# Kernel tuning notes

Measured on AMD Instinct MI355X. Metric: run time of the kernel, lower is better.

Reference implementation:

```python
import jax, jax.numpy as jnp
import numpy as np

B, T, C, H = 8, 2048, 2048, 128  # batch, seq, n_embd, head_size


def setup_inputs() -> dict:
    key = jax.random.key(0)
    kx, kq, kk, kv = jax.random.split(key, 4)
    x = jax.random.normal(kx, (B, T, C), dtype=jnp.float32)
    # Linear(n_embd, head_size, bias=False); stored as [in, out] so x @ W matches x @ weight.T in torch
    Wq = jax.random.normal(kq, (C, H), dtype=jnp.float32) * 0.02
    Wk = jax.random.normal(kk, (C, H), dtype=jnp.float32) * 0.02
    Wv = jax.random.normal(kv, (C, H), dtype=jnp.float32) * 0.02
    return {"x": x, "Wq": Wq, "Wk": Wk, "Wv": Wv}


def reference(x, Wq, Wk, Wv):
    # Single-head scaled dot-product attention (mask=False path of the module)
    q = jnp.einsum("btc,ch->bth", x, Wq)  # [B,T,H]
    k = jnp.einsum("btc,ch->bth", x, Wk)
    v = jnp.einsum("btc,ch->bth", x, Wv)
    scale = k.shape[-1] ** -0.5
    wei = jnp.einsum("bqh,bkh->bqk", q, k) * scale  # [B,T,T]
    wei = jax.nn.softmax(wei, axis=-1)
    out = jnp.einsum("bqk,bkh->bqh", wei, v)  # [B,T,H]
    return out
```

## Files before the change

### kernel.cpp

```cpp
#include <hip/hip_runtime.h>
#include <hip/hip_bf16.h>

typedef __attribute__((ext_vector_type(8))) short short8;
typedef __attribute__((ext_vector_type(4))) float f32x4;

#define MFMA16(a, b, c) __builtin_amdgcn_mfma_f32_16x16x32_bf16((a), (b), (c), 0, 0, 0)

__device__ __forceinline__ unsigned short f2bf(float f) {
    __hip_bfloat16 h = __float2bfloat16(f);
    return __builtin_bit_cast(unsigned short, h);
}

__device__ __forceinline__ short8 cvt8(f32x4 a, f32x4 b) {
    short8 r;
    r[0] = (short)f2bf(a[0]); r[1] = (short)f2bf(a[1]);
    r[2] = (short)f2bf(a[2]); r[3] = (short)f2bf(a[3]);
    r[4] = (short)f2bf(b[0]); r[5] = (short)f2bf(b[1]);
    r[6] = (short)f2bf(b[2]); r[7] = (short)f2bf(b[3]);
    return r;
}

__global__ __launch_bounds__(256) void wt_kernel(const float* __restrict__ Wq,
                                                 const float* __restrict__ Wk,
                                                 const float* __restrict__ Wv,
                                                 unsigned short* __restrict__ Wt) {
    __shared__ float T[64][65];
    const int j = blockIdx.z;
    const float* W = (j == 0) ? Wq : (j == 1) ? Wk : Wv;
    const int c0 = blockIdx.x * 64;
    const int h0 = blockIdx.y * 64;
    const int tid = threadIdx.x;

#pragma unroll
    for (int i = 0; i < 4; i++) {
        const int cc = tid + 256 * i;
        const int r = cc >> 4;
        const int q4 = (cc & 15) * 4;
        f32x4 vv = *(const f32x4*)(W + (size_t)(c0 + r) * 128 + h0 + q4);
        T[r][q4 + 0] = vv[0]; T[r][q4 + 1] = vv[1];
        T[r][q4 + 2] = vv[2]; T[r][q4 + 3] = vv[3];
    }
    __syncthreads();
#pragma unroll
    for (int i = 0; i < 2; i++) {
        const int oc = tid + 256 * i;
        const int hr = oc >> 3;
        const int c8 = (oc & 7) * 8;
        short8 r;
#pragma unroll
        for (int e = 0; e < 8; e++) r[e] = (short)f2bf(T[c8 + e][hr]);
        *(short8*)(Wt + (size_t)j * (128 * 2048) + (size_t)(h0 + hr) * 2048 + c0 + c8) = r;
    }
}

__global__ __launch_bounds__(256) void qkv_gemm(const float* __restrict__ x,
                                                const unsigned short* __restrict__ Wt,
                                                unsigned short* __restrict__ qkv) {
    constexpr int LDT = 72;
    __shared__ __align__(16) unsigned short As[128 * LDT];
    __shared__ __align__(16) unsigned short Bs[128 * LDT];

    const int tid = threadIdx.x;
    const int l = tid & 63;
    const int w = tid >> 6;
    const int wr = w >> 1, wc = w & 1;
    const int bn = blockIdx.x;
    const int bm = blockIdx.y;
    const int lrow = l & 15, lk = (l >> 4) * 8;

    const float* xA = x + (size_t)bm * 128 * 2048;
    const unsigned short* Wb = Wt + (size_t)bn * (128 * 2048);
    unsigned short* outp = qkv + (size_t)bn * (16384 * 128);

    const f32x4 fzero = {0.f, 0.f, 0.f, 0.f};
    f32x4 acc[4][4];
#pragma unroll
    for (int mt = 0; mt < 4; mt++)
#pragma unroll
        for (int nt = 0; nt < 4; nt++) acc[mt][nt] = fzero;

    for (int kt = 0; kt < 32; kt++) {
        __syncthreads();
#pragma unroll
        for (int i = 0; i < 4; i++) {
            const int c = tid + 256 * i;
            const int m = c >> 3;
            const int k0 = (c & 7) * 8;
            const float* src = xA + (size_t)m * 2048 + kt * 64 + k0;
            f32x4 f0 = *(const f32x4*)(src);
            f32x4 f1 = *(const f32x4*)(src + 4);
            *(short8*)&As[m * LDT + k0] = cvt8(f0, f1);
        }
#pragma unroll
        for (int i = 0; i < 4; i++) {
            const int c = tid + 256 * i;
            const int n = c >> 3;
            const int k0 = (c & 7) * 8;
            short8 bv = *(const short8*)(Wb + (size_t)n * 2048 + kt * 64 + k0);
            *(short8*)&Bs[n * LDT + k0] = bv;
        }
        __syncthreads();
#pragma unroll
        for (int ks = 0; ks < 2; ks++) {
            short8 af[4], bfr[4];
#pragma unroll
            for (int mt = 0; mt < 4; mt++)
                af[mt] = *(const short8*)&As[(wr * 64 + mt * 16 + lrow) * LDT + ks * 32 + lk];
#pragma unroll
            for (int nt = 0; nt < 4; nt++)
                bfr[nt] = *(const short8*)&Bs[(wc * 64 + nt * 16 + lrow) * LDT + ks * 32 + lk];
#pragma unroll
            for (int mt = 0; mt < 4; mt++)
#pragma unroll
                for (int nt = 0; nt < 4; nt++)
                    acc[mt][nt] = MFMA16(af[mt], bfr[nt], acc[mt][nt]);
        }
    }

    const float scale = (bn == 0) ? 0.08838834764831845f : 1.0f;
#pragma unroll
    for (int mt = 0; mt < 4; mt++)
#pragma unroll
        for (int nt = 0; nt < 4; nt++)
#pragma unroll
            for (int r = 0; r < 4; r++) {
                const int row = bm * 128 + wr * 64 + mt * 16 + (l >> 4) * 4 + r;
                const int col = wc * 64 + nt * 16 + lrow;
                outp[(size_t)row * 128 + col] = f2bf(acc[mt][nt][r] * scale);
            }
}

template <bool SPLIT>
__global__ __launch_bounds__(256) void attn_kernel_t(const unsigned short* __restrict__ q,
                                                     const unsigned short* __restrict__ k,
                                                     const unsigned short* __restrict__ v,
                                                     float* __restrict__ Oout,
                                                     float* __restrict__ Ml) {
    constexpr int KS = 136;
    constexpr int VS = 88;
    constexpr int PS = 88;
    __shared__ __align__(16) unsigned short Ks[64 * KS];
    __shared__ __align__(16) unsigned short Vt[128 * VS];
    __shared__ __align__(16) unsigned short Psh[64 * PS];

    const int tid = threadIdx.x;
    const int l = tid & 63;
    const int w = tid >> 6;
    const int qt = blockIdx.x;
    const int b = blockIdx.y;
    const int s = SPLIT ? blockIdx.z : 0;
    const int kv_beg = SPLIT ? s * 11 : 0;
    const int kv_end = SPLIT ? ((s == 2) ? 32 : kv_beg + 11) : 32;
    const int lrow = l & 15, g = l >> 4, lk = g * 8;

    const size_t qbase = ((size_t)b * 2048 + qt * 64 + w * 16 + lrow) * 128;
    short8 qf[4];
#pragma unroll
    for (int ks = 0; ks < 4; ks++) qf[ks] = *(const short8*)(q + qbase + ks * 32 + lk);

    const f32x4 fzero = {0.f, 0.f, 0.f, 0.f};
    float m_r[4], l_r[4];
    f32x4 oacc[8];
#pragma unroll
    for (int r = 0; r < 4; r++) { m_r[r] = -1e30f; l_r[r] = 0.f; }
#pragma unroll
    for (int d = 0; d < 8; d++) oacc[d] = fzero;

    const int skey = tid & 63;
    const int sd = (tid >> 6) * 8;

    for (int kv = kv_beg; kv < kv_end; kv++) {
        __syncthreads();
        const size_t kvbase = ((size_t)b * 2048 + kv * 64 + skey) * 128;
#pragma unroll
        for (int jj = 0; jj < 4; jj++) {
            const int d0 = sd + jj * 32;
            short8 kvv = *(const short8*)(k + kvbase + d0);
            *(short8*)&Ks[skey * KS + d0] = kvv;
        }
#pragma unroll
        for (int jj = 0; jj < 4; jj++) {
            const int d0 = sd + jj * 32;
            short8 vv = *(const short8*)(v + kvbase + d0);
#pragma unroll
            for (int e = 0; e < 8; e++)
                Vt[(d0 + e) * VS + skey] = (unsigned short)vv[e];
        }
        __syncthreads();

        f32x4 sv[4];
#pragma unroll
        for (int nt = 0; nt < 4; nt++) sv[nt] = fzero;
#pragma unroll
        for (int ks = 0; ks < 4; ks++)
#pragma unroll
            for (int nt = 0; nt < 4; nt++) {
                short8 kf = *(const short8*)&Ks[(nt * 16 + lrow) * KS + ks * 32 + lk];
                sv[nt] = MFMA16(qf[ks], kf, sv[nt]);
            }

        float sf[4];
#pragma unroll
        for (int r = 0; r < 4; r++) {
            float tmax = fmaxf(fmaxf(sv[0][r], sv[1][r]), fmaxf(sv[2][r], sv[3][r]));
#pragma unroll
            for (int mk = 8; mk >= 1; mk >>= 1) tmax = fmaxf(tmax, __shfl_xor(tmax, mk));
            const float mnew = fmaxf(m_r[r], tmax);
            sf[r] = __expf(m_r[r] - mnew);
            m_r[r] = mnew;
            float psum = 0.f;
#pragma unroll
            for (int nt = 0; nt < 4; nt++) {
                const float p = __expf(sv[nt][r] - mnew);
                sv[nt][r] = p;
                psum += p;
            }
#pragma unroll
            for (int mk = 8; mk >= 1; mk >>= 1) psum += __shfl_xor(psum, mk);
            l_r[r] = l_r[r] * sf[r] + psum;
        }
#pragma unroll
        for (int d = 0; d < 8; d++)
#pragma unroll
            for (int r = 0; r < 4; r++) oacc[d][r] *= sf[r];

#pragma unroll
        for (int nt = 0; nt < 4; nt++)
#pragma unroll
            for (int r = 0; r < 4; r++)
                Psh[(w * 16 + g * 4 + r) * PS + nt * 16 + lrow] = f2bf(sv[nt][r]);
        __syncthreads();

#pragma unroll
        for (int ks2 = 0; ks2 < 2; ks2++) {
            short8 pa = *(const short8*)&Psh[(w * 16 + lrow) * PS + ks2 * 32 + lk];
#pragma unroll
            for (int dt = 0; dt < 8; dt++) {
                short8 vbf = *(const short8*)&Vt[(dt * 16 + lrow) * VS + ks2 * 32 + lk];
                oacc[dt] = MFMA16(pa, vbf, oacc[dt]);
            }
        }
    }

#pragma unroll
    for (int r = 0; r < 4; r++) {
        const int rowi = b * 2048 + qt * 64 + w * 16 + g * 4 + r;
        if (SPLIT) {
            const size_t obase = ((size_t)s * 16384 + rowi) * 128;
#pragma unroll
            for (int dt = 0; dt < 8; dt++)
                Oout[obase + dt * 16 + lrow] = oacc[dt][r];
            if (lrow == 0) {
                const size_t mb = ((size_t)s * 16384 + rowi) * 2;
                Ml[mb] = m_r[r];
                Ml[mb + 1] = l_r[r];
            }
        } else {
            const float inv = 1.0f / l_r[r];
#pragma unroll
            for (int dt = 0; dt < 8; dt++)
                Oout[(size_t)rowi * 128 + dt * 16 + lrow] = oacc[dt][r] * inv;
        }
    }
}

__global__ __launch_bounds__(256) void attn_merge(const float* __restrict__ Oacc,
                                                  const float* __restrict__ Ml,
                                                  float* __restrict__ out) {
    const int row = blockIdx.x * 2 + (threadIdx.x >> 7);
    const int c = threadIdx.x & 127;
    const float m0 = Ml[(size_t)(0 * 16384 + row) * 2], l0 = Ml[(size_t)(0 * 16384 + row) * 2 + 1];
    const float m1 = Ml[(size_t)(1 * 16384 + row) * 2], l1 = Ml[(size_t)(1 * 16384 + row) * 2 + 1];
    const float m2 = Ml[(size_t)(2 * 16384 + row) * 2], l2 = Ml[(size_t)(2 * 16384 + row) * 2 + 1];
    const float M = fmaxf(m0, fmaxf(m1, m2));
    const float w0 = __expf(m0 - M), w1 = __expf(m1 - M), w2 = __expf(m2 - M);
    const float D = w0 * l0 + w1 * l1 + w2 * l2;
    const float o = w0 * Oacc[(size_t)(0 * 16384 + row) * 128 + c] +
                    w1 * Oacc[(size_t)(1 * 16384 + row) * 128 + c] +
                    w2 * Oacc[(size_t)(2 * 16384 + row) * 128 + c];
    out[(size_t)row * 128 + c] = o / D;
}

extern "C" void kernel_launch(void* const* d_in, const int* in_sizes, int n_in,
                              void* d_out, int out_size, void* d_ws, size_t ws_size,
                              hipStream_t stream) {
    const float* x  = (const float*)d_in[0];
    const float* Wq = (const float*)d_in[1];
    const float* Wk = (const float*)d_in[2];
    const float* Wv = (const float*)d_in[3];
    float* out = (float*)d_out;

    unsigned short* ws = (unsigned short*)d_ws;
    unsigned short* qb = ws;
    unsigned short* kb = qb + (size_t)16384 * 128;
    unsigned short* vb = kb + (size_t)16384 * 128;
    unsigned short* Wt = vb + (size_t)16384 * 128;
    float* Oacc = (float*)(Wt + (size_t)3 * 128 * 2048);
    float* Ml = Oacc + (size_t)3 * 16384 * 128;
    const size_t ws_need = (size_t)((char*)(Ml + (size_t)3 * 16384 * 2) - (char*)d_ws);

    hipLaunchKernelGGL(wt_kernel, dim3(32, 2, 3), dim3(256), 0, stream, Wq, Wk, Wv, Wt);
    hipLaunchKernelGGL(qkv_gemm, dim3(3, 128), dim3(256), 0, stream, x, Wt, qb);
    if (ws_size >= ws_need) {
        hipLaunchKernelGGL((attn_kernel_t<true>), dim3(32, 8, 3), dim3(256), 0, stream,
                           qb, kb, vb, Oacc, Ml);
        hipLaunchKernelGGL(attn_merge, dim3(8192), dim3(256), 0, stream, Oacc, Ml, out);
    } else {
        hipLaunchKernelGGL((attn_kernel_t<false>), dim3(32, 8), dim3(256), 0, stream,
                           qb, kb, vb, out, (float*)nullptr);
    }
}
```

Baseline: 295.9 us.

## Double-buffer QKV GEMM with direct global-to-LDS loads and swizzled B tile

Rewrites the QKV projection GEMM to use 64-row M tiles (768 blocks), double-buffered LDS, and prefetch of the next k-tile during MFMA compute. The B tile is loaded with global_load_lds straight into an XOR-swizzled LDS layout, while the fp32 x tile is held in registers and converted to bf16 after compute. It also remaps block IDs so blocks sharing an x row tile are grouped, and sets launch bounds for 3 blocks per CU. The aim is to hide global load latency and cut the per-iteration sync count, at the cost of more LDS and a smaller per-block tile.

Measured after the change: 293.0 us. No clear change (-1.0%).

```diff
diff --git a/kernel.cpp b/kernel.cpp
--- a/kernel.cpp
+++ b/kernel.cpp
@@ -5,6 +5,11 @@
 typedef __attribute__((ext_vector_type(4))) float f32x4;
 
 #define MFMA16(a, b, c) __builtin_amdgcn_mfma_f32_16x16x32_bf16((a), (b), (c), 0, 0, 0)
+
+#define GLOAD_LDS16(gp, lp)                                                            \
+    __builtin_amdgcn_global_load_lds(                                                  \
+        (const __attribute__((address_space(1))) unsigned int*)(gp),                   \
+        (__attribute__((address_space(3))) unsigned int*)(lp), 16, 0, 0)
 
 __device__ __forceinline__ unsigned short f2bf(float f) {
     __hip_bfloat16 h = __float2bfloat16(f);
@@ -53,78 +58,112 @@
     }
 }
 
-__global__ __launch_bounds__(256) void qkv_gemm(const float* __restrict__ x,
-                                                const unsigned short* __restrict__ Wt,
-                                                unsigned short* __restrict__ qkv) {
-    constexpr int LDT = 72;
-    __shared__ __align__(16) unsigned short As[128 * LDT];
-    __shared__ __align__(16) unsigned short Bs[128 * LDT];
+__global__ __launch_bounds__(256, 3) void qkv_gemm(const float* __restrict__ x,
+                                                   const unsigned short* __restrict__ Wt,
+                                                   unsigned short* __restrict__ qkv) {
+    constexpr int LDA = 72;
+    __shared__ __align__(16) unsigned short As[2][64 * LDA];
+    __shared__ __align__(16) unsigned short Bs[2][128 * 64];
 
     const int tid = threadIdx.x;
     const int l = tid & 63;
     const int w = tid >> 6;
     const int wr = w >> 1, wc = w & 1;
-    const int bn = blockIdx.x;
-    const int bm = blockIdx.y;
-    const int lrow = l & 15, lk = (l >> 4) * 8;
-
-    const float* xA = x + (size_t)bm * 128 * 2048;
+    const int lrow = l & 15, g = l >> 4, lk = g * 8;
+
+    const int p = blockIdx.x;
+    const int wg = (p & 7) * 96 + (p >> 3);
+    const int bn = wg % 3;
+    const int bm = wg / 3;
+
+    const float* xA = x + (size_t)bm * 64 * 2048;
     const unsigned short* Wb = Wt + (size_t)bn * (128 * 2048);
     unsigned short* outp = qkv + (size_t)bn * (16384 * 128);
 
+    const int rowA = tid >> 2;
+    const int quad = tid & 3;
+    const float* srcA0 = xA + (size_t)rowA * 2048 + quad * 16;
+
+    const int brow_base = (w << 5) + (l >> 3);
+    const int bsw = ((l >> 3) & 7) << 4;
+    const int bslot = (l & 7) << 4;
+    const int bsrc_off = ((bslot ^ bsw) >> 1);
+
     const f32x4 fzero = {0.f, 0.f, 0.f, 0.f};
-    f32x4 acc[4][4];
-#pragma unroll
-    for (int mt = 0; mt < 4; mt++)
+    f32x4 acc[2][4];
+#pragma unroll
+    for (int mt = 0; mt < 2; mt++)
 #pragma unroll
         for (int nt = 0; nt < 4; nt++) acc[mt][nt] = fzero;
 
+#pragma unroll
+    for (int i = 0; i < 4; i++) {
+        const int row = brow_base + (i << 3);
+        GLOAD_LDS16(Wb + (size_t)row * 2048 + bsrc_off,
+                    &Bs[0][(w << 11) + (i << 9)]);
+    }
+    {
+        f32x4 a0 = *(const f32x4*)(srcA0);
+        f32x4 a1 = *(const f32x4*)(srcA0 + 4);
+        f32x4 a2 = *(const f32x4*)(srcA0 + 8);
+        f32x4 a3 = *(const f32x4*)(srcA0 + 12);
+        *(short8*)&As[0][rowA * LDA + quad * 16] = cvt8(a0, a1);
+        *(short8*)&As[0][rowA * LDA + quad * 16 + 8] = cvt8(a2, a3);
+    }
+    __syncthreads();
+
+    int cur = 0;
     for (int kt = 0; kt < 32; kt++) {
-        __syncthreads();
-#pragma unroll
-        for (int i = 0; i < 4; i++) {
-            const int c = tid + 256 * i;
-            const int m = c >> 3;
-            const int k0 = (c & 7) * 8;
-            const float* src = xA + (size_t)m * 2048 + kt * 64 + k0;
-            f32x4 f0 = *(const f32x4*)(src);
-            f32x4 f1 = *(const f32x4*)(src + 4);
-            *(short8*)&As[m * LDT + k0] = cvt8(f0, f1);
-        }
-#pragma unroll
-        for (int i = 0; i < 4; i++) {
-            const int c = tid + 256 * i;
-            const int n = c >> 3;
-            const int k0 = (c & 7) * 8;
-            short8 bv = *(const short8*)(Wb + (size_t)n * 2048 + kt * 64 + k0);
-            *(short8*)&Bs[n * LDT + k0] = bv;
-        }
-        __syncthreads();
+        f32x4 a0, a1, a2, a3;
+        if (kt < 31) {
+#pragma unroll
+            for (int i = 0; i < 4; i++) {
+                const int row = brow_base + (i << 3);
+                GLOAD_LDS16(Wb + (size_t)row * 2048 + (kt + 1) * 64 + bsrc_off,
+                            &Bs[cur ^ 1][(w << 11) + (i << 9)]);
+            }
+            const float* sA = srcA0 + (kt + 1) * 64;
+            a0 = *(const f32x4*)(sA);
+            a1 = *(const f32x4*)(sA + 4);
+            a2 = *(const f32x4*)(sA + 8);
+            a3 = *(const f32x4*)(sA + 12);
+        }
+
 #pragma unroll
         for (int ks = 0; ks < 2; ks++) {
-            short8 af[4], bfr[4];
-#pragma unroll
-            for (int mt = 0; mt < 4; mt++)
-                af[mt] = *(const short8*)&As[(wr * 64 + mt * 16 + lrow) * LDT + ks * 32 + lk];
-#pragma unroll
-            for (int nt = 0; nt < 4; nt++)
-                bfr[nt] = *(const short8*)&Bs[(wc * 64 + nt * 16 + lrow) * LDT + ks * 32 + lk];
-#pragma unroll
-            for (int mt = 0; mt < 4; mt++)
+            short8 af[2], bfr[4];
+#pragma unroll
+            for (int mt = 0; mt < 2; mt++)
+                af[mt] = *(const short8*)&As[cur][(wr * 32 + mt * 16 + lrow) * LDA + ks * 32 + lk];
+#pragma unroll
+            for (int nt = 0; nt < 4; nt++) {
+                const int n = wc * 64 + nt * 16 + lrow;
+                const int kbyte = (ks * 64 + g * 16) ^ ((n & 7) << 4);
+                bfr[nt] = *(const short8*)&Bs[cur][n * 64 + (kbyte >> 1)];
+            }
+#pragma unroll
+            for (int mt = 0; mt < 2; mt++)
 #pragma unroll
                 for (int nt = 0; nt < 4; nt++)
                     acc[mt][nt] = MFMA16(af[mt], bfr[nt], acc[mt][nt]);
         }
+
+        if (kt < 31) {
+            *(short8*)&As[cur ^ 1][rowA * LDA + quad * 16] = cvt8(a0, a1);
+            *(short8*)&As[cur ^ 1][rowA * LDA + quad * 16 + 8] = cvt8(a2, a3);
+        }
+        __syncthreads();
+        cur ^= 1;
     }
 
     const float scale = (bn == 0) ? 0.08838834764831845f : 1.0f;
 #pragma unroll
-    for (int mt = 0; mt < 4; mt++)
+    for (int mt = 0; mt < 2; mt++)
 #pragma unroll
         for (int nt = 0; nt < 4; nt++)
 #pragma unroll
             for (int r = 0; r < 4; r++) {
-                const int row = bm * 128 + wr * 64 + mt * 16 + (l >> 4) * 4 + r;
+                const int row = bm * 64 + wr * 32 + mt * 16 + g * 4 + r;
                 const int col = wc * 64 + nt * 16 + lrow;
                 outp[(size_t)row * 128 + col] = f2bf(acc[mt][nt][r] * scale);
             }
@@ -211,9 +250,9 @@
             float psum = 0.f;
 #pragma unroll
             for (int nt = 0; nt < 4; nt++) {
-                const float p = __expf(sv[nt][r] - mnew);
-                sv[nt][r] = p;
-                psum += p;
+                const float pp = __expf(sv[nt][r] - mnew);
+                sv[nt][r] = pp;
+                psum += pp;
             }
 #pragma unroll
             for (int mk = 8; mk >= 1; mk >>= 1) psum += __shfl_xor(psum, mk);
@@ -300,7 +339,7 @@
     const size_t ws_need = (size_t)((char*)(Ml + (size_t)3 * 16384 * 2) - (char*)d_ws);
 
     hipLaunchKernelGGL(wt_kernel, dim3(32, 2, 3), dim3(256), 0, stream, Wq, Wk, Wv, Wt);
-    hipLaunchKernelGGL(qkv_gemm, dim3(3, 128), dim3(256), 0, stream, x, Wt, qb);
+    hipLaunchKernelGGL(qkv_gemm, dim3(768), dim3(256), 0, stream, x, Wt, qb);
     if (ws_size >= ws_need) {
         hipLaunchKernelGGL((attn_kernel_t<true>), dim3(32, 8, 3), dim3(256), 0, stream,
                            qb, kb, vb, Oacc, Ml);
```

## Prefetch next K/V tile in attention and stream QKV GEMM operands without LDS

Applied to the files above, without the earlier changes.

The attention kernel now loads the next K/V tile into registers while the current tile's QK^T, softmax and PV run. The tile is written to shared memory after a barrier at the end of each iteration. The barrier between the P write and the P read is dropped, because each wave reads only its own P rows. The QKV projection GEMM drops its shared-memory staging: each wave loads its own fp32 x rows and bf16 weight fragments straight from global memory. Its 2D grid becomes a 1D grid with a swizzle that keeps the three projections of a row block on the same XCD to share L2, and both kernels get a minimum-occupancy launch bound. The risks are higher register pressure and redundant global weight loads across waves, which now rely on cache hits.

After: 407.5 us. 37.7% more time.

```diff
diff --git a/kernel.cpp b/kernel.cpp
--- a/kernel.cpp
+++ b/kernel.cpp
@@ -53,89 +53,73 @@
     }
 }
 
-__global__ __launch_bounds__(256) void qkv_gemm(const float* __restrict__ x,
-                                                const unsigned short* __restrict__ Wt,
-                                                unsigned short* __restrict__ qkv) {
-    constexpr int LDT = 72;
-    __shared__ __align__(16) unsigned short As[128 * LDT];
-    __shared__ __align__(16) unsigned short Bs[128 * LDT];
-
+__global__ __launch_bounds__(256, 3) void qkv_gemm(const float* __restrict__ x,
+                                                   const unsigned short* __restrict__ Wt,
+                                                   unsigned short* __restrict__ qkv) {
     const int tid = threadIdx.x;
     const int l = tid & 63;
     const int w = tid >> 6;
-    const int wr = w >> 1, wc = w & 1;
-    const int bn = blockIdx.x;
-    const int bm = blockIdx.y;
-    const int lrow = l & 15, lk = (l >> 4) * 8;
-
-    const float* xA = x + (size_t)bm * 128 * 2048;
+    const int lrow = l & 15, g = l >> 4;
+
+    const int p = blockIdx.x;
+    const int wg = (p & 7) * 48 + (p >> 3);
+    const int bn = wg % 3;
+    const int bm = wg / 3;
+
     const unsigned short* Wb = Wt + (size_t)bn * (128 * 2048);
     unsigned short* outp = qkv + (size_t)bn * (16384 * 128);
 
+    const float* xb = x + ((size_t)bm * 128 + w * 32 + lrow) * 2048 + g * 8;
+    const unsigned short* wbl = Wb + (size_t)lrow * 2048 + g * 8;
+
     const f32x4 fzero = {0.f, 0.f, 0.f, 0.f};
-    f32x4 acc[4][4];
-#pragma unroll
-    for (int mt = 0; mt < 4; mt++)
-#pragma unroll
-        for (int nt = 0; nt < 4; nt++) acc[mt][nt] = fzero;
-
-    for (int kt = 0; kt < 32; kt++) {
-        __syncthreads();
-#pragma unroll
-        for (int i = 0; i < 4; i++) {
-            const int c = tid + 256 * i;
-            const int m = c >> 3;
-            const int k0 = (c & 7) * 8;
-            const float* src = xA + (size_t)m * 2048 + kt * 64 + k0;
-            f32x4 f0 = *(const f32x4*)(src);
-            f32x4 f1 = *(const f32x4*)(src + 4);
-            *(short8*)&As[m * LDT + k0] = cvt8(f0, f1);
-        }
-#pragma unroll
-        for (int i = 0; i < 4; i++) {
-            const int c = tid + 256 * i;
-            const int n = c >> 3;
-            const int k0 = (c & 7) * 8;
-            short8 bv = *(const short8*)(Wb + (size_t)n * 2048 + kt * 64 + k0);
-            *(short8*)&Bs[n * LDT + k0] = bv;
-        }
-        __syncthreads();
-#pragma unroll
-        for (int ks = 0; ks < 2; ks++) {
-            short8 af[4], bfr[4];
-#pragma unroll
-            for (int mt = 0; mt < 4; mt++)
-                af[mt] = *(const short8*)&As[(wr * 64 + mt * 16 + lrow) * LDT + ks * 32 + lk];
-#pragma unroll
-            for (int nt = 0; nt < 4; nt++)
-                bfr[nt] = *(const short8*)&Bs[(wc * 64 + nt * 16 + lrow) * LDT + ks * 32 + lk];
-#pragma unroll
-            for (int mt = 0; mt < 4; mt++)
-#pragma unroll
-                for (int nt = 0; nt < 4; nt++)
-                    acc[mt][nt] = MFMA16(af[mt], bfr[nt], acc[mt][nt]);
-        }
+    f32x4 acc[2][8];
+#pragma unroll
+    for (int mt = 0; mt < 2; mt++)
+#pragma unroll
+        for (int nt = 0; nt < 8; nt++) acc[mt][nt] = fzero;
+
+#pragma unroll 4
+    for (int kt = 0; kt < 64; kt++) {
+        const int k0 = kt * 32;
+        short8 af[2];
+#pragma unroll
+        for (int mt = 0; mt < 2; mt++) {
+            const float* sa = xb + mt * (16 * 2048) + k0;
+            f32x4 f0 = *(const f32x4*)(sa);
+            f32x4 f1 = *(const f32x4*)(sa + 4);
+            af[mt] = cvt8(f0, f1);
+        }
+        short8 bf[8];
+#pragma unroll
+        for (int nt = 0; nt < 8; nt++)
+            bf[nt] = *(const short8*)(wbl + nt * (16 * 2048) + k0);
+#pragma unroll
+        for (int mt = 0; mt < 2; mt++)
+#pragma unroll
+            for (int nt = 0; nt < 8; nt++)
+                acc[mt][nt] = MFMA16(af[mt], bf[nt], acc[mt][nt]);
     }
 
     const float scale = (bn == 0) ? 0.08838834764831845f : 1.0f;
 #pragma unroll
-    for (int mt = 0; mt < 4; mt++)
-#pragma unroll
-        for (int nt = 0; nt < 4; nt++)
+    for (int mt = 0; mt < 2; mt++)
+#pragma unroll
+        for (int nt = 0; nt < 8; nt++)
 #pragma unroll
             for (int r = 0; r < 4; r++) {
-                const int row = bm * 128 + wr * 64 + mt * 16 + (l >> 4) * 4 + r;
-                const int col = wc * 64 + nt * 16 + lrow;
+                const int row = bm * 128 + w * 32 + mt * 16 + g * 4 + r;
+                const int col = nt * 16 + lrow;
                 outp[(size_t)row * 128 + col] = f2bf(acc[mt][nt][r] * scale);
             }
 }
 
 template <bool SPLIT>
-__global__ __launch_bounds__(256) void attn_kernel_t(const unsigned short* __restrict__ q,
-                                                     const unsigned short* __restrict__ k,
-                                                     const unsigned short* __restrict__ v,
-                                                     float* __restrict__ Oout,
-                                                     float* __restrict__ Ml) {
+__global__ __launch_bounds__(256, 3) void attn_kernel_t(const unsigned short* __restrict__ q,
+                                                        const unsigned short* __restrict__ k,
+                                                        const unsigned short* __restrict__ v,
+                                                        float* __restrict__ Oout,
+                                                        float* __restrict__ Ml) {
     constexpr int KS = 136;
     constexpr int VS = 88;
     constexpr int PS = 88;
@@ -169,24 +153,35 @@
     const int skey = tid & 63;
     const int sd = (tid >> 6) * 8;
 
+    short8 kr[4], vr[4];
+    {
+        const size_t kvbase = ((size_t)b * 2048 + kv_beg * 64 + skey) * 128;
+#pragma unroll
+        for (int jj = 0; jj < 4; jj++) {
+            kr[jj] = *(const short8*)(k + kvbase + sd + jj * 32);
+            vr[jj] = *(const short8*)(v + kvbase + sd + jj * 32);
+        }
+    }
+#pragma unroll
+    for (int jj = 0; jj < 4; jj++) {
+        const int d0 = sd + jj * 32;
+        *(short8*)&Ks[skey * KS + d0] = kr[jj];
+#pragma unroll
+        for (int e = 0; e < 8; e++)
+            Vt[(d0 + e) * VS + skey] = (unsigned short)vr[jj][e];
+    }
+    __syncthreads();
+
     for (int kv = kv_beg; kv < kv_end; kv++) {
-        __syncthreads();
-        const size_t kvbase = ((size_t)b * 2048 + kv * 64 + skey) * 128;
-#pragma unroll
-        for (int jj = 0; jj < 4; jj++) {
-            const int d0 = sd + jj * 32;
-            short8 kvv = *(const short8*)(k + kvbase + d0);
-            *(short8*)&Ks[skey * KS + d0] = kvv;
-        }
-#pragma unroll
-        for (int jj = 0; jj < 4; jj++) {
-            const int d0 = sd + jj * 32;
-            short8 vv = *(const short8*)(v + kvbase + d0);
-#pragma unroll
-            for (int e = 0; e < 8; e++)
-                Vt[(d0 + e) * VS + skey] = (unsigned short)vv[e];
-        }
-        __syncthreads();
+        const bool has_next = (kv + 1 < kv_end);
+        if (has_next) {
+            const size_t kvbase = ((size_t)b * 2048 + (kv + 1) * 64 + skey) * 128;
+#pragma unroll
+            for (int jj = 0; jj < 4; jj++) {
+                kr[jj] = *(const short8*)(k + kvbase + sd + jj * 32);
+                vr[jj] = *(const short8*)(v + kvbase + sd + jj * 32);
+            }
+        }
 
         f32x4 sv[4];
 #pragma unroll
@@ -211,9 +206,9 @@
             float psum = 0.f;
 #pragma unroll
             for (int nt = 0; nt < 4; nt++) {
-                const float p = __expf(sv[nt][r] - mnew);
-                sv[nt][r] = p;
-                psum += p;
+                const float pp = __expf(sv[nt][r] - mnew);
+                sv[nt][r] = pp;
+                psum += pp;
             }
 #pragma unroll
             for (int mk = 8; mk >= 1; mk >>= 1) psum += __shfl_xor(psum, mk);
@@ -229,7 +224,6 @@
 #pragma unroll
             for (int r = 0; r < 4; r++)
                 Psh[(w * 16 + g * 4 + r) * PS + nt * 16 + lrow] = f2bf(sv[nt][r]);
-        __syncthreads();
 
 #pragma unroll
         for (int ks2 = 0; ks2 < 2; ks2++) {
@@ -240,6 +234,19 @@
                 oacc[dt] = MFMA16(pa, vbf, oacc[dt]);
             }
         }
+
+        __syncthreads();
+        if (has_next) {
+#pragma unroll
+            for (int jj = 0; jj < 4; jj++) {
+                const int d0 = sd + jj * 32;
+                *(short8*)&Ks[skey * KS + d0] = kr[jj];
+#pragma unroll
+                for (int e = 0; e < 8; e++)
+                    Vt[(d0 + e) * VS + skey] = (unsigned short)vr[jj][e];
+            }
+        }
+        __syncthreads();
     }
 
 #pragma unroll
@@ -300,7 +307,7 @@
     const size_t ws_need = (size_t)((char*)(Ml + (size_t)3 * 16384 * 2) - (char*)d_ws);
 
     hipLaunchKernelGGL(wt_kernel, dim3(32, 2, 3), dim3(256), 0, stream, Wq, Wk, Wv, Wt);
-    hipLaunchKernelGGL(qkv_gemm, dim3(3, 128), dim3(256), 0, stream, x, Wt, qb);
+    hipLaunchKernelGGL(qkv_gemm, dim3(384), dim3(256), 0, stream, x, Wt, qb);
     if (ws_size >= ws_need) {
         hipLaunchKernelGGL((attn_kernel_t<true>), dim3(32, 8, 3), dim3(256), 0, stream,
                            qb, kb, vb, Oacc, Ml);
```
